# Kernel optimization log

Measured on AMD Instinct MI355X. Metric: run time of the kernel, lower is better.

The kernel has to match this reference:

```python
import jax, jax.numpy as jnp
import numpy as np

SIGMA = 0.1  # kernel-point influence radius (KPConv linear correlation)


def setup_inputs() -> dict:
    key = jax.random.key(0)
    k1, k2, k3, k4, k5 = jax.random.split(key, 5)
    N, K, KP, CIN, COUT = 65536, 32, 15, 64, 128
    pos = jax.random.uniform(k1, (N, 3), dtype=jnp.float32)
    feats = jax.random.normal(k2, (N, CIN), dtype=jnp.float32)
    kernel_points = jax.random.normal(k3, (KP, 3), dtype=jnp.float32) * 0.05
    weights = jax.random.normal(k4, (KP, CIN, COUT), dtype=jnp.float32) / np.sqrt(KP * CIN)
    neighbors = jax.random.randint(k5, (N, K), 0, N, dtype=jnp.int64)
    return {"pos": pos, "feats": feats, "kernel_points": kernel_points,
            "weights": weights, "neighbors": neighbors}


def reference(pos, feats, kernel_points, weights, neighbors):
    # pos: [N,3], feats: [N,Cin], kernel_points: [Kp,3],
    # weights: [Kp,Cin,Cout], neighbors: [N,K] int
    neigh_pos = pos[neighbors]                      # [N,K,3] irregular gather
    rel = neigh_pos - pos[:, None, :]               # [N,K,3]
    # distance from each relative neighbor offset to each kernel point
    d = rel[:, :, None, :] - kernel_points[None, None, :, :]   # [N,K,Kp,3]
    dist = jnp.sqrt(jnp.sum(d * d, axis=-1))        # [N,K,Kp]
    infl = jnp.maximum(0.0, 1.0 - dist / SIGMA)     # linear correlation
    neigh_feat = feats[neighbors]                   # [N,K,Cin] irregular gather
    # per-kernel-point weighted neighbor aggregation, then projection
    weighted = jnp.einsum('njk,njc->nkc', infl, neigh_feat)    # [N,Kp,Cin]
    out = jnp.einsum('nkc,kcd->nd', weighted, weights)         # [N,Cout]
    return out
```

## Files before the change

### kernel.cpp

```cpp
#include <hip/hip_runtime.h>

#define NPTS  65536
#define KNB   32
#define KPn   15
#define CIN   64
#define COUT  128
#define MPTS  16
#define THREADS 512
#define WSTRIDE 968
#define BCAP  48
#define RCAP  96
#define NTILE 8
#define KSTEPS 30
#define WELEMS (NTILE * KSTEPS * 64 * 8)

typedef __attribute__((ext_vector_type(8))) short short8;
typedef __attribute__((ext_vector_type(4))) float f32x4;

__device__ __forceinline__ unsigned int f2bf(float f) {
    union { float f; unsigned int i; } v; v.f = f;
    return (v.i + 0x7fffu + ((v.i >> 16) & 1u)) >> 16;
}
__device__ __forceinline__ float bflo(unsigned int u) {
    union { unsigned int i; float f; } v; v.i = u << 16; return v.f;
}
__device__ __forceinline__ float bfhi(unsigned int u) {
    union { unsigned int i; float f; } v; v.i = u & 0xFFFF0000u; return v.f;
}

__global__ void wtrans_kernel(const float* __restrict__ w,
                              const float* __restrict__ kpts,
                              unsigned short* __restrict__ wTf,
                              float4* __restrict__ kpq_out) {
    const int d = blockIdx.x * 256 + threadIdx.x;
    if (d < WELEMS) {
        const int j    = d & 7;
        const int lane = (d >> 3) & 63;
        const int ks   = (d >> 9) % KSTEPS;
        const int t    = d / (KSTEPS * 512);
        const int f    = ks * 32 + (lane >> 4) * 8 + j;
        const int cg   = f / 120;
        const int rem  = f - cg * 120;
        const int orig = (rem >> 3) * 64 + cg * 8 + (rem & 7);
        const int n    = t * 16 + (lane & 15);
        wTf[d] = (unsigned short)f2bf(w[(size_t)orig * COUT + n]);
    }
    if (blockIdx.x == 0 && threadIdx.x < 16) {
        const int k = threadIdx.x;
        if (k < KPn) {
            const float x = kpts[k * 3 + 0];
            const float y = kpts[k * 3 + 1];
            const float z = kpts[k * 3 + 2];
            kpq_out[k] = make_float4(x, y, z, x * x + y * y + z * z);
        } else {
            float mx = 0.f;
            for (int i = 0; i < KPn; ++i) {
                const float x = kpts[i * 3 + 0];
                const float y = kpts[i * 3 + 1];
                const float z = kpts[i * 3 + 2];
                mx = fmaxf(mx, x * x + y * y + z * z);
            }
            const float R = 0.1f + sqrtf(mx);
            kpq_out[15] = make_float4(R * R, 0.f, 0.f, 0.f);
        }
    }
}

__global__ __launch_bounds__(THREADS, 8) void kpconv_kernel(
    const float* __restrict__ pos,
    const float* __restrict__ feats,
    const unsigned short* __restrict__ wTf,
    const float4* __restrict__ kpq_in,
    const int*   __restrict__ neighbors,
    float*       __restrict__ out)
{
    __shared__ __align__(16) unsigned short wl[MPTS * WSTRIDE];
    __shared__ __align__(16) unsigned short sfeat[RCAP * CIN];
    __shared__ unsigned int  bpk[MPTS][BCAP];
    __shared__ int    bcnt[MPTS];
    __shared__ float  cposf[MPTS * 3];
    __shared__ float4 kpq[KPn];
    __shared__ float  rlx[RCAP], rly[RCAP], rlz[RCAP], rld[RCAP];
    __shared__ unsigned int rsl[RCAP];
    __shared__ int    nact;

    const int tid = threadIdx.x;
    const int n0  = blockIdx.x * MPTS;

    const int   p0  = tid >> 5;
    const int   nb0 = neighbors[(size_t)n0 * KNB + tid];
    const float qx  = pos[(size_t)nb0 * 3 + 0];
    const float qy  = pos[(size_t)nb0 * 3 + 1];
    const float qz  = pos[(size_t)nb0 * 3 + 2];
    const float R2  = kpq_in[15].x;

    if (tid < KPn) kpq[tid] = kpq_in[tid];
    if (tid < MPTS) bcnt[tid] = 0;
    if (tid == 0) nact = 0;
    if (tid < MPTS * 3) cposf[tid] = pos[(size_t)n0 * 3 + tid];
    __syncthreads();

    {
        const float rx = qx - cposf[p0 * 3 + 0];
        const float ry = qy - cposf[p0 * 3 + 1];
        const float rz = qz - cposf[p0 * 3 + 2];
        const float d2r = rx * rx + ry * ry + rz * rz;
        if (d2r < R2) {
            const int idx = atomicAdd(&nact, 1);
            if (idx < RCAP) {
                rlx[idx] = rx; rly[idx] = ry; rlz[idx] = rz; rld[idx] = d2r;
                rsl[idx] = ((unsigned int)p0 << 16) | (unsigned int)nb0;
            }
        }
    }
    __syncthreads();

    {
        const int E      = min(nact, RCAP);
        const int staged = E * 16;
        for (int u = tid; u < staged * 2; u += THREADS) {
            if (u < staged) {
                const int e = u >> 4;
                const int c = u & 15;
                const int nb = (int)(rsl[e] & 0xFFFFu);
                const float4 f = *(const float4*)(feats + (size_t)nb * CIN + c * 4);
                const unsigned int lo = f2bf(f.x) | (f2bf(f.y) << 16);
                const unsigned int hi = f2bf(f.z) | (f2bf(f.w) << 16);
                *(uint2*)(sfeat + e * CIN + c * 4) = make_uint2(lo, hi);
            } else {
                const int v = u - staged;
                const int e = v >> 4;
                const int k = v & 15;
                if (k < KPn) {
                    const float4 kp  = kpq[k];
                    const float  d2r = rld[e];
                    const float dot = rlx[e] * kp.x + rly[e] * kp.y + rlz[e] * kp.z;
                    if (dot > 0.5f * (d2r - 0.01f + kp.w)) {
                        const float d2 = fmaxf(d2r - 2.f * dot + kp.w, 0.f);
                        const float w  = 1.0f - 10.0f * sqrtf(d2);
                        const unsigned int wq = (unsigned int)(w * 4095.0f + 0.5f);
                        const int p = (int)(rsl[e] >> 16);
                        const int idx = atomicAdd(&bcnt[p], 1);
                        if (idx < BCAP)
                            bpk[p][idx] = ((unsigned int)e << 16) |
                                          ((unsigned int)k << 12) | wq;
                    }
                }
            }
        }
    }
    __syncthreads();

    #pragma unroll
    for (int it = 0; it < 4; ++it) {
        const int wi = tid + it * THREADS;
        const int cg = wi & 7;
        const int k  = (wi >> 3) & 15;
        const int p  = wi >> 7;
        if (k < KPn) {
            float a0=0.f,a1=0.f,a2=0.f,a3=0.f,a4=0.f,a5=0.f,a6=0.f,a7=0.f;
            const int cnt = min(bcnt[p], BCAP);
            for (int e = 0; e < cnt; ++e) {
                const unsigned int id = bpk[p][e];
                if (((id >> 12) & 15u) == (unsigned int)k) {
                    const float wv = (float)(id & 4095u) * (1.0f / 4095.0f);
                    const uint4 vf = *(const uint4*)(sfeat + (id >> 16) * CIN + cg * 8);
                    a0 += wv * bflo(vf.x); a1 += wv * bfhi(vf.x);
                    a2 += wv * bflo(vf.y); a3 += wv * bfhi(vf.y);
                    a4 += wv * bflo(vf.z); a5 += wv * bfhi(vf.z);
                    a6 += wv * bflo(vf.w); a7 += wv * bfhi(vf.w);
                }
            }
            uint4 u;
            u.x = f2bf(a0) | (f2bf(a1) << 16);
            u.y = f2bf(a2) | (f2bf(a3) << 16);
            u.z = f2bf(a4) | (f2bf(a5) << 16);
            u.w = f2bf(a6) | (f2bf(a7) << 16);
            *(uint4*)(wl + p * WSTRIDE + cg * 120 + k * 8) = u;
        }
    }
    __syncthreads();

    {
        const int wave = tid >> 6;
        const int lane = tid & 63;
        const int m    = lane & 15;
        const int q    = lane >> 4;

        f32x4 acc = {0.f, 0.f, 0.f, 0.f};
        const unsigned short* ap = wl + m * WSTRIDE + q * 8;
        const short8* bp = (const short8*)wTf + (size_t)wave * KSTEPS * 64 + lane;

        #pragma unroll 5
        for (int ks = 0; ks < KSTEPS; ++ks, ap += 32) {
            const short8 a = *(const short8*)ap;
            const short8 b = bp[ks * 64];
            acc = __builtin_amdgcn_mfma_f32_16x16x32_bf16(a, b, acc, 0, 0, 0);
        }

        const int c = wave * 16 + m;
        #pragma unroll
        for (int r = 0; r < 4; ++r)
            out[(size_t)(n0 + q * 4 + r) * COUT + c] = acc[r];
    }
}

extern "C" void kernel_launch(void* const* d_in, const int* in_sizes, int n_in,
                              void* d_out, int out_size, void* d_ws, size_t ws_size,
                              hipStream_t stream) {
    const float* pos       = (const float*)d_in[0];
    const float* feats     = (const float*)d_in[1];
    const float* kpts      = (const float*)d_in[2];
    const float* weights   = (const float*)d_in[3];
    const int*   neighbors = (const int*)d_in[4];
    float*       out       = (float*)d_out;
    unsigned short* wTf    = (unsigned short*)d_ws;
    float4* kpq            = (float4*)((char*)d_ws + WELEMS * 2);

    wtrans_kernel<<<(WELEMS + 255) / 256, 256, 0, stream>>>(weights, kpts, wTf, kpq);
    kpconv_kernel<<<NPTS / MPTS, THREADS, 0, stream>>>(
        pos, feats, wTf, kpq, neighbors, out);
}
```

Measured before the change: 138.9 us.

## Compute neighbor aggregation with MFMA over dense influence matrix chunks

Replaces the sparse bucketed scalar aggregation (atomic bucket lists and per-thread scan loops) with a dense bf16 influence matrix per chunk of 32 active neighbors, multiplied against transposed staged features using MFMA. Shared memory is pooled and aliased between phases, and the weight layout is changed to pad kernel points to 16 so the projection uses 32 K-steps. This removes divergent scalar loops and atomics but adds zero-fill passes, extra barriers per chunk, and wasted MFMA work on zero padding.

Measured after the change: 146.1 us. +5.2%, slower.

```diff
diff --git a/kernel.cpp b/kernel.cpp
--- a/kernel.cpp
+++ b/kernel.cpp
@@ -7,12 +7,23 @@
 #define COUT  128
 #define MPTS  16
 #define THREADS 512
-#define WSTRIDE 968
-#define BCAP  48
 #define RCAP  96
+#define CHUNK 32
+#define ESTR  40
+#define WSTR  1032
+#define KSTEPS 32
 #define NTILE 8
-#define KSTEPS 30
 #define WELEMS (NTILE * KSTEPS * 64 * 8)
+
+#define OFF_INFL   0
+#define OFF_SFT    20480
+#define ZERO_B16   ((20480 + 5120) / 16)
+#define OFF_RLX    25600
+#define OFF_RLY    (OFF_RLX + 384)
+#define OFF_RLZ    (OFF_RLY + 384)
+#define OFF_RLD    (OFF_RLZ + 384)
+#define OFF_RSL    (OFF_RLD + 384)
+#define POOL_BYTES (MPTS * WSTR * 2)
 
 typedef __attribute__((ext_vector_type(8))) short short8;
 typedef __attribute__((ext_vector_type(4))) float f32x4;
@@ -21,11 +32,10 @@
     union { float f; unsigned int i; } v; v.f = f;
     return (v.i + 0x7fffu + ((v.i >> 16) & 1u)) >> 16;
 }
-__device__ __forceinline__ float bflo(unsigned int u) {
-    union { unsigned int i; float f; } v; v.i = u << 16; return v.f;
-}
-__device__ __forceinline__ float bfhi(unsigned int u) {
-    union { unsigned int i; float f; } v; v.i = u & 0xFFFF0000u; return v.f;
+__device__ __forceinline__ unsigned int cvt_pk_bf16(float lo, float hi) {
+    unsigned int r;
+    asm volatile("v_cvt_pk_bf16_f32 %0, %1, %2" : "=v"(r) : "v"(lo), "v"(hi));
+    return r;
 }
 
 __global__ void wtrans_kernel(const float* __restrict__ w,
@@ -36,14 +46,15 @@
     if (d < WELEMS) {
         const int j    = d & 7;
         const int lane = (d >> 3) & 63;
-        const int ks   = (d >> 9) % KSTEPS;
-        const int t    = d / (KSTEPS * 512);
-        const int f    = ks * 32 + (lane >> 4) * 8 + j;
-        const int cg   = f / 120;
-        const int rem  = f - cg * 120;
-        const int orig = (rem >> 3) * 64 + cg * 8 + (rem & 7);
+        const int ks   = (d >> 9) & 31;
+        const int t    = d >> 14;
+        const int f    = ks * 32 + ((lane >> 4) & 3) * 8 + j;
+        const int k    = f & 15;
+        const int c    = f >> 4;
         const int n    = t * 16 + (lane & 15);
-        wTf[d] = (unsigned short)f2bf(w[(size_t)orig * COUT + n]);
+        wTf[d] = (k < KPn)
+            ? (unsigned short)f2bf(w[((size_t)k * CIN + c) * COUT + n])
+            : (unsigned short)0;
     }
     if (blockIdx.x == 0 && threadIdx.x < 16) {
         const int k = threadIdx.x;
@@ -74,18 +85,26 @@
     const int*   __restrict__ neighbors,
     float*       __restrict__ out)
 {
-    __shared__ __align__(16) unsigned short wl[MPTS * WSTRIDE];
-    __shared__ __align__(16) unsigned short sfeat[RCAP * CIN];
-    __shared__ unsigned int  bpk[MPTS][BCAP];
-    __shared__ int    bcnt[MPTS];
+    __shared__ __align__(16) unsigned char pool[POOL_BYTES];
     __shared__ float  cposf[MPTS * 3];
     __shared__ float4 kpq[KPn];
-    __shared__ float  rlx[RCAP], rly[RCAP], rlz[RCAP], rld[RCAP];
-    __shared__ unsigned int rsl[RCAP];
     __shared__ int    nact;
 
-    const int tid = threadIdx.x;
-    const int n0  = blockIdx.x * MPTS;
+    unsigned short* const wl     = (unsigned short*)pool;
+    unsigned short* const infl   = (unsigned short*)(pool + OFF_INFL);
+    unsigned short* const sfeatT = (unsigned short*)(pool + OFF_SFT);
+    float*          const rlx    = (float*)(pool + OFF_RLX);
+    float*          const rly    = (float*)(pool + OFF_RLY);
+    float*          const rlz    = (float*)(pool + OFF_RLZ);
+    float*          const rld    = (float*)(pool + OFF_RLD);
+    unsigned int*   const rsl    = (unsigned int*)(pool + OFF_RSL);
+
+    const int tid  = threadIdx.x;
+    const int n0   = blockIdx.x * MPTS;
+    const int lane = tid & 63;
+    const int wv   = tid >> 6;
+    const int m    = lane & 15;
+    const int q    = lane >> 4;
 
     const int   p0  = tid >> 5;
     const int   nb0 = neighbors[(size_t)n0 * KNB + tid];
@@ -95,7 +114,6 @@
     const float R2  = kpq_in[15].x;
 
     if (tid < KPn) kpq[tid] = kpq_in[tid];
-    if (tid < MPTS) bcnt[tid] = 0;
     if (tid == 0) nact = 0;
     if (tid < MPTS * 3) cposf[tid] = pos[(size_t)n0 * 3 + tid];
     __syncthreads();
@@ -115,93 +133,101 @@
     }
     __syncthreads();
 
+    const int E   = min(nact, RCAP);
+    const int nch = (E + CHUNK - 1) >> 5;
+
+    f32x4 acc[2][4];
+    #pragma unroll
+    for (int i = 0; i < 2; ++i)
+        #pragma unroll
+        for (int nt = 0; nt < 4; ++nt)
+            acc[i][nt] = (f32x4){0.f, 0.f, 0.f, 0.f};
+
+    for (int ch = 0; ch < nch; ++ch) {
+        {
+            uint4* zp = (uint4*)pool;
+            #pragma unroll
+            for (int i = 0; i < 4; ++i) {
+                const int idx = tid + i * THREADS;
+                if (idx < ZERO_B16) zp[idx] = make_uint4(0u, 0u, 0u, 0u);
+            }
+        }
+        __syncthreads();
+
+        const int ce = min(E - ch * CHUNK, CHUNK);
+
+        {
+            const int el = tid & 31;
+            const int c4 = tid >> 5;
+            if (el < ce) {
+                const int nb = (int)(rsl[ch * CHUNK + el] & 0xFFFFu);
+                const float4 f = *(const float4*)(feats + (size_t)nb * CIN + c4 * 4);
+                sfeatT[(c4 * 4 + 0) * ESTR + el] = (unsigned short)f2bf(f.x);
+                sfeatT[(c4 * 4 + 1) * ESTR + el] = (unsigned short)f2bf(f.y);
+                sfeatT[(c4 * 4 + 2) * ESTR + el] = (unsigned short)f2bf(f.z);
+                sfeatT[(c4 * 4 + 3) * ESTR + el] = (unsigned short)f2bf(f.w);
+            }
+        }
+        if (tid < ce * 16) {
+            const int el = tid >> 4;
+            const int k  = tid & 15;
+            if (k < KPn) {
+                const int e = ch * CHUNK + el;
+                const float4 kp  = kpq[k];
+                const float  d2r = rld[e];
+                const float dot = rlx[e] * kp.x + rly[e] * kp.y + rlz[e] * kp.z;
+                if (dot > 0.5f * (d2r - 0.01f + kp.w)) {
+                    const float d2 = fmaxf(d2r - 2.f * dot + kp.w, 0.f);
+                    const float w  = 1.0f - 10.0f * sqrtf(d2);
+                    const int p = (int)(rsl[e] >> 16);
+                    infl[(p * 16 + k) * ESTR + el] = (unsigned short)f2bf(w);
+                }
+            }
+        }
+        __syncthreads();
+
+        {
+            const short8 aA = *(const short8*)(infl + ((wv * 2 + 0) * 16 + m) * ESTR + q * 8);
+            const short8 aB = *(const short8*)(infl + ((wv * 2 + 1) * 16 + m) * ESTR + q * 8);
+            #pragma unroll
+            for (int nt = 0; nt < 4; ++nt) {
+                const short8 b = *(const short8*)(sfeatT + (nt * 16 + m) * ESTR + q * 8);
+                acc[0][nt] = __builtin_amdgcn_mfma_f32_16x16x32_bf16(aA, b, acc[0][nt], 0, 0, 0);
+                acc[1][nt] = __builtin_amdgcn_mfma_f32_16x16x32_bf16(aB, b, acc[1][nt], 0, 0, 0);
+            }
+        }
+        __syncthreads();
+    }
+
+    #pragma unroll
+    for (int i = 0; i < 2; ++i) {
+        const int p = wv * 2 + i;
+        #pragma unroll
+        for (int nt = 0; nt < 4; ++nt) {
+            const int c = nt * 16 + m;
+            unsigned short* wp = wl + p * WSTR + c * 16 + q * 4;
+            *(unsigned int*)(wp)     = cvt_pk_bf16(acc[i][nt][0], acc[i][nt][1]);
+            *(unsigned int*)(wp + 2) = cvt_pk_bf16(acc[i][nt][2], acc[i][nt][3]);
+        }
+    }
+    __syncthreads();
+
     {
-        const int E      = min(nact, RCAP);
-        const int staged = E * 16;
-        for (int u = tid; u < staged * 2; u += THREADS) {
-            if (u < staged) {
-                const int e = u >> 4;
-                const int c = u & 15;
-                const int nb = (int)(rsl[e] & 0xFFFFu);
-                const float4 f = *(const float4*)(feats + (size_t)nb * CIN + c * 4);
-                const unsigned int lo = f2bf(f.x) | (f2bf(f.y) << 16);
-                const unsigned int hi = f2bf(f.z) | (f2bf(f.w) << 16);
-                *(uint2*)(sfeat + e * CIN + c * 4) = make_uint2(lo, hi);
-            } else {
-                const int v = u - staged;
-                const int e = v >> 4;
-                const int k = v & 15;
-                if (k < KPn) {
-                    const float4 kp  = kpq[k];
-                    const float  d2r = rld[e];
-                    const float dot = rlx[e] * kp.x + rly[e] * kp.y + rlz[e] * kp.z;
-                    if (dot > 0.5f * (d2r - 0.01f + kp.w)) {
-                        const float d2 = fmaxf(d2r - 2.f * dot + kp.w, 0.f);
-                        const float w  = 1.0f - 10.0f * sqrtf(d2);
-                        const unsigned int wq = (unsigned int)(w * 4095.0f + 0.5f);
-                        const int p = (int)(rsl[e] >> 16);
-                        const int idx = atomicAdd(&bcnt[p], 1);
-                        if (idx < BCAP)
-                            bpk[p][idx] = ((unsigned int)e << 16) |
-                                          ((unsigned int)k << 12) | wq;
-                    }
-                }
-            }
-        }
-    }
-    __syncthreads();
-
-    #pragma unroll
-    for (int it = 0; it < 4; ++it) {
-        const int wi = tid + it * THREADS;
-        const int cg = wi & 7;
-        const int k  = (wi >> 3) & 15;
-        const int p  = wi >> 7;
-        if (k < KPn) {
-            float a0=0.f,a1=0.f,a2=0.f,a3=0.f,a4=0.f,a5=0.f,a6=0.f,a7=0.f;
-            const int cnt = min(bcnt[p], BCAP);
-            for (int e = 0; e < cnt; ++e) {
-                const unsigned int id = bpk[p][e];
-                if (((id >> 12) & 15u) == (unsigned int)k) {
-                    const float wv = (float)(id & 4095u) * (1.0f / 4095.0f);
-                    const uint4 vf = *(const uint4*)(sfeat + (id >> 16) * CIN + cg * 8);
-                    a0 += wv * bflo(vf.x); a1 += wv * bfhi(vf.x);
-                    a2 += wv * bflo(vf.y); a3 += wv * bfhi(vf.y);
-                    a4 += wv * bflo(vf.z); a5 += wv * bfhi(vf.z);
-                    a6 += wv * bflo(vf.w); a7 += wv * bfhi(vf.w);
-                }
-            }
-            uint4 u;
-            u.x = f2bf(a0) | (f2bf(a1) << 16);
-            u.y = f2bf(a2) | (f2bf(a3) << 16);
-            u.z = f2bf(a4) | (f2bf(a5) << 16);
-            u.w = f2bf(a6) | (f2bf(a7) << 16);
-            *(uint4*)(wl + p * WSTRIDE + cg * 120 + k * 8) = u;
-        }
-    }
-    __syncthreads();
-
-    {
-        const int wave = tid >> 6;
-        const int lane = tid & 63;
-        const int m    = lane & 15;
-        const int q    = lane >> 4;
-
-        f32x4 acc = {0.f, 0.f, 0.f, 0.f};
-        const unsigned short* ap = wl + m * WSTRIDE + q * 8;
-        const short8* bp = (const short8*)wTf + (size_t)wave * KSTEPS * 64 + lane;
-
-        #pragma unroll 5
+        f32x4 o = {0.f, 0.f, 0.f, 0.f};
+        const unsigned short* ap = wl + m * WSTR + q * 8;
+        const short8* bp = (const short8*)wTf + (size_t)wv * KSTEPS * 64 + lane;
+
+        #pragma unroll 4
         for (int ks = 0; ks < KSTEPS; ++ks, ap += 32) {
             const short8 a = *(const short8*)ap;
             const short8 b = bp[ks * 64];
-            acc = __builtin_amdgcn_mfma_f32_16x16x32_bf16(a, b, acc, 0, 0, 0);
-        }
-
-        const int c = wave * 16 + m;
+            o = __builtin_amdgcn_mfma_f32_16x16x32_bf16(a, b, o, 0, 0, 0);
+        }
+
+        const int c = wv * 16 + m;
         #pragma unroll
         for (int r = 0; r < 4; ++r)
-            out[(size_t)(n0 + q * 4 + r) * COUT + c] = acc[r];
+            out[(size_t)(n0 + q * 4 + r) * COUT + c] = o[r];
     }
 }
 
@@ -217,7 +243,7 @@
     unsigned short* wTf    = (unsigned short*)d_ws;
     float4* kpq            = (float4*)((char*)d_ws + WELEMS * 2);
 
-    wtrans_kernel<<<(WELEMS + 255) / 256, 256, 0, stream>>>(weights, kpts, wTf, kpq);
+    wtrans_kernel<<<WELEMS / 256, 256, 0, stream>>>(weights, kpts, wTf, kpq);
     kpconv_kernel<<<NPTS / MPTS, THREADS, 0, stream>>>(
         pos, feats, wTf, kpq, neighbors, out);
 }
```
